# Optimization experiments

Measured on AMD Instinct MI355X. Metric: run time of the kernel, lower is better.

The kernel has to match this reference:

```python
import jax, jax.numpy as jnp
import numpy as np

IN_DIM, OUT_DIM = 256, 64
N_D, N_G, N_C, N_S = 100000, 50000, 50000, 20000
E = 1000000
ALPHA = 0.2  # LeakyReLU negative slope


def setup_inputs() -> dict:
    key = jax.random.key(0)
    ks = jax.random.split(key, 14)
    scale = float(np.sqrt(6.0 / (IN_DIM + OUT_DIM)) * 1.414)
    scale_w = float(np.sqrt(6.0 / (4 * OUT_DIM + OUT_DIM)) * 1.414)
    return {
        "disease_feats": jax.random.normal(ks[0], (N_D, IN_DIM), jnp.float32),
        "gene_feats": jax.random.normal(ks[1], (N_G, IN_DIM), jnp.float32),
        "chemical_feats": jax.random.normal(ks[2], (N_C, IN_DIM), jnp.float32),
        "species_feats": jax.random.normal(ks[3], (N_S, IN_DIM), jnp.float32),
        "P_disease": jax.random.uniform(ks[4], (IN_DIM, OUT_DIM), jnp.float32, -scale, scale),
        "P_gene": jax.random.uniform(ks[5], (IN_DIM, OUT_DIM), jnp.float32, -scale, scale),
        "P_chemical": jax.random.uniform(ks[6], (IN_DIM, OUT_DIM), jnp.float32, -scale, scale),
        "P_species": jax.random.uniform(ks[7], (IN_DIM, OUT_DIM), jnp.float32, -scale, scale),
        "W_GDCD": jax.random.uniform(ks[8], (4 * OUT_DIM, OUT_DIM), jnp.float32, -scale_w, scale_w),
        "idx_d0": jax.random.randint(ks[9], (E,), 0, N_D, jnp.int32),
        "idx_d1": jax.random.randint(ks[10], (E,), 0, N_D, jnp.int32),
        "idx_g": jax.random.randint(ks[11], (E,), 0, N_G, jnp.int32),
        "idx_c": jax.random.randint(ks[12], (E,), 0, N_C, jnp.int32),
    }


def reference(disease_feats, gene_feats, chemical_feats, species_feats,
              P_disease, P_gene, P_chemical, P_species, W_GDCD,
              idx_d0, idx_d1, idx_g, idx_c):
    # Per-type linear projections (pattern 'GDCD')
    f_disease = disease_feats @ P_disease      # [N_D, out]
    f_gene = gene_feats @ P_gene               # [N_G, out]
    f_chemical = chemical_feats @ P_chemical   # [N_C, out]
    # f_species is computed by the torch code but unused for GDCD; omitted (dead code under jit)
    # Gather per-instance rows and concat -> [E, 4*out]
    concat = jnp.concatenate(
        [f_disease[idx_d0], f_disease[idx_d1], f_gene[idx_g], f_chemical[idx_c]], axis=1)
    instance = concat @ W_GDCD                 # [E, out]
    return jax.nn.leaky_relu(instance, negative_slope=ALPHA)
```

## Files before the change

kernel.cpp:

```cpp
#include <hip/hip_runtime.h>

typedef __attribute__((ext_vector_type(8))) short          short8;
typedef __attribute__((ext_vector_type(4))) float          f32x4;
typedef __attribute__((ext_vector_type(8))) unsigned short ushort8;

#define ALPHA 0.2f

__device__ __forceinline__ unsigned short f2bf(float f) {
    union { float f; unsigned int u; } x; x.f = f;
    unsigned int u = x.u;
    u += 0x7fffu + ((u >> 16) & 1u);
    return (unsigned short)(u >> 16);
}
__device__ __forceinline__ float bf2f(unsigned short u) {
    union { unsigned int i; float f; } x; x.i = ((unsigned int)u) << 16;
    return x.f;
}

__global__ __launch_bounds__(256)
void make_frags(const float* __restrict__ Pd, const float* __restrict__ Pg,
                const float* __restrict__ Pc, const float* __restrict__ W,
                unsigned short* __restrict__ fd, unsigned short* __restrict__ fg,
                unsigned short* __restrict__ fc) {
    int t = blockIdx.x * 256 + threadIdx.x;
    int local, NCT, mbase; unsigned short* dst;
    if (t < 32768)      { local = t;         NCT = 8; dst = fd; mbase = 0; }
    else if (t < 49152) { local = t - 32768; NCT = 4; dst = fg; mbase = 2; }
    else                { local = t - 49152; NCT = 4; dst = fc; mbase = 3; }
    int j    = local & 7;
    int lane = (local >> 3) & 63;
    int ct   = (local >> 9) & (NCT - 1);
    int kk   = local >> (9 + (NCT == 8 ? 3 : 2));
    int k = kk * 32 + ((lane >> 4) << 3) + j;
    int c = ct * 16 + (lane & 15);
    int m, cc; const float* P;
    if (NCT == 8) { m = (c < 64) ? 0 : 1; cc = c & 63; P = Pd; }
    else          { m = mbase;            cc = c;      P = (mbase == 2) ? Pg : Pc; }
    float acc = 0.f;
    #pragma unroll 8
    for (int q = 0; q < 64; ++q)
        acc += P[k * 64 + q] * W[(m * 64 + q) * 64 + cc];
    dst[local] = f2bf(acc);
}

#define TPW 2

template <int NCT>
__device__ __forceinline__
void proj_body(const float* __restrict__ feats,
               const unsigned short* __restrict__ bfrag,
               unsigned short* __restrict__ g, int ntiles, int blk,
               unsigned short* blds) {
    const int t = threadIdx.x;
    #pragma unroll
    for (int i = 0; i < NCT; ++i) {
        int off = (i * 512 + t) * 8;
        *(int4*)&blds[off] = *(const int4*)&bfrag[off];
    }
    __syncthreads();

    const int wid = t >> 6, lane = t & 63;
    const int C = NCT * 16;

    #pragma unroll
    for (int it = 0; it < TPW; ++it) {
        const int tile = (blk * 8 + wid) * TPW + it;
        if (tile >= ntiles) return;

        const int row = tile * 16 + (lane & 15);
        const float* arow = feats + (size_t)row * 256 + ((lane >> 4) * 8);

        f32x4 acc[NCT];
        #pragma unroll
        for (int ct = 0; ct < NCT; ++ct) acc[ct] = (f32x4){0.f, 0.f, 0.f, 0.f};

        #pragma unroll
        for (int kk = 0; kk < 8; ++kk) {
            f32x4 v0 = __builtin_nontemporal_load((const f32x4*)(arow + kk * 32));
            f32x4 v1 = __builtin_nontemporal_load((const f32x4*)(arow + kk * 32 + 4));
            short8 a;
            a[0] = (short)f2bf(v0[0]); a[1] = (short)f2bf(v0[1]);
            a[2] = (short)f2bf(v0[2]); a[3] = (short)f2bf(v0[3]);
            a[4] = (short)f2bf(v1[0]); a[5] = (short)f2bf(v1[1]);
            a[6] = (short)f2bf(v1[2]); a[7] = (short)f2bf(v1[3]);
            #pragma unroll
            for (int ct = 0; ct < NCT; ++ct) {
                short8 b = *(const short8*)&blds[((kk * NCT + ct) * 64 + lane) * 8];
                acc[ct] = __builtin_amdgcn_mfma_f32_16x16x32_bf16(a, b, acc[ct], 0, 0, 0);
            }
        }

        const int rbase = tile * 16 + (lane >> 4) * 4;
        const int cbase = lane & 15;
        #pragma unroll
        for (int ct = 0; ct < NCT; ++ct) {
            #pragma unroll
            for (int j = 0; j < 4; ++j)
                g[(size_t)(rbase + j) * C + ct * 16 + cbase] = f2bf(acc[ct][j]);
        }
    }
}

__global__ __launch_bounds__(512)
void proj_all(const float* __restrict__ featd, const float* __restrict__ featg,
              const float* __restrict__ featc,
              const unsigned short* __restrict__ fragd,
              const unsigned short* __restrict__ fragg,
              const unsigned short* __restrict__ fragc,
              unsigned short* __restrict__ g_d, unsigned short* __restrict__ g_g,
              unsigned short* __restrict__ g_c,
              int nbd, int nbg, int td, int tg, int tc) {
    __shared__ unsigned short blds[32768];
    int b = blockIdx.x;
    if (b < nbd)            proj_body<8>(featd, fragd, g_d, td, b,             blds);
    else if (b < nbd + nbg) proj_body<4>(featg, fragg, g_g, tg, b - nbd,       blds);
    else                    proj_body<4>(featc, fragc, g_c, tc, b - nbd - nbg, blds);
}

__global__ __launch_bounds__(256)
void gather_kernel(const unsigned short* __restrict__ g_d,
                   const unsigned short* __restrict__ g_g,
                   const unsigned short* __restrict__ g_c,
                   const int* __restrict__ i0, const int* __restrict__ i1,
                   const int* __restrict__ ig, const int* __restrict__ ic,
                   float* __restrict__ out, int E, int Eh) {
    int tid = blockIdx.x * 256 + threadIdx.x;
    int e0 = tid >> 3;
    if (e0 >= Eh) return;
    int q = tid & 3;
    q = tid & 7;
    int e1 = e0 + Eh;
    bool has1 = e1 < E;

    int a0  = __builtin_nontemporal_load(i0 + e0);
    int b0  = __builtin_nontemporal_load(i1 + e0);
    int gi0 = __builtin_nontemporal_load(ig + e0);
    int ci0 = __builtin_nontemporal_load(ic + e0);
    int a1 = 0, b1 = 0, gi1 = 0, ci1 = 0;
    if (has1) {
        a1  = __builtin_nontemporal_load(i0 + e1);
        b1  = __builtin_nontemporal_load(i1 + e1);
        gi1 = __builtin_nontemporal_load(ig + e1);
        ci1 = __builtin_nontemporal_load(ic + e1);
    }

    ushort8 v0 = *(const ushort8*)(g_d + (size_t)a0  * 128 + q * 8);
    ushort8 v1 = *(const ushort8*)(g_d + (size_t)b0  * 128 + 64 + q * 8);
    ushort8 v2 = *(const ushort8*)(g_g + (size_t)gi0 * 64 + q * 8);
    ushort8 v3 = *(const ushort8*)(g_c + (size_t)ci0 * 64 + q * 8);
    ushort8 w0, w1, w2, w3;
    if (has1) {
        w0 = *(const ushort8*)(g_d + (size_t)a1  * 128 + q * 8);
        w1 = *(const ushort8*)(g_d + (size_t)b1  * 128 + 64 + q * 8);
        w2 = *(const ushort8*)(g_g + (size_t)gi1 * 64 + q * 8);
        w3 = *(const ushort8*)(g_c + (size_t)ci1 * 64 + q * 8);
    }

    f32x4 r0, r1;
    #pragma unroll
    for (int j = 0; j < 4; ++j) {
        float s = bf2f(v0[j]) + bf2f(v1[j]) + bf2f(v2[j]) + bf2f(v3[j]);
        r0[j] = s >= 0.f ? s : s * ALPHA;
        float u = bf2f(v0[j + 4]) + bf2f(v1[j + 4]) + bf2f(v2[j + 4]) + bf2f(v3[j + 4]);
        r1[j] = u >= 0.f ? u : u * ALPHA;
    }
    float* o0 = out + (size_t)e0 * 64 + q * 8;
    __builtin_nontemporal_store(r0, (f32x4*)o0);
    __builtin_nontemporal_store(r1, (f32x4*)(o0 + 4));

    if (has1) {
        #pragma unroll
        for (int j = 0; j < 4; ++j) {
            float s = bf2f(w0[j]) + bf2f(w1[j]) + bf2f(w2[j]) + bf2f(w3[j]);
            r0[j] = s >= 0.f ? s : s * ALPHA;
            float u = bf2f(w0[j + 4]) + bf2f(w1[j + 4]) + bf2f(w2[j + 4]) + bf2f(w3[j + 4]);
            r1[j] = u >= 0.f ? u : u * ALPHA;
        }
        float* o1 = out + (size_t)e1 * 64 + q * 8;
        __builtin_nontemporal_store(r0, (f32x4*)o1);
        __builtin_nontemporal_store(r1, (f32x4*)(o1 + 4));
    }
}

extern "C" void kernel_launch(void* const* d_in, const int* in_sizes, int n_in,
                              void* d_out, int out_size, void* d_ws, size_t ws_size,
                              hipStream_t stream) {
    const float* feats_d = (const float*)d_in[0];
    const float* feats_g = (const float*)d_in[1];
    const float* feats_c = (const float*)d_in[2];
    const float* Pd = (const float*)d_in[4];
    const float* Pg = (const float*)d_in[5];
    const float* Pc = (const float*)d_in[6];
    const float* W  = (const float*)d_in[8];
    const int* i0 = (const int*)d_in[9];
    const int* i1 = (const int*)d_in[10];
    const int* ig = (const int*)d_in[11];
    const int* ic = (const int*)d_in[12];
    float* out = (float*)d_out;

    const int N_D = in_sizes[0] / 256;
    const int N_G = in_sizes[1] / 256;
    const int N_C = in_sizes[2] / 256;
    const int E   = in_sizes[9];

    char* ws = (char*)d_ws;
    unsigned short* fd  = (unsigned short*)ws;
    unsigned short* fg  = (unsigned short*)(ws + 65536);
    unsigned short* fc  = (unsigned short*)(ws + 98304);
    unsigned short* g_d = (unsigned short*)(ws + 131072);
    unsigned short* g_g = g_d + (size_t)N_D * 128;
    unsigned short* g_c = g_g + (size_t)N_G * 64;

    make_frags<<<256, 256, 0, stream>>>(Pd, Pg, Pc, W, fd, fg, fc);

    int td = N_D / 16, tg = N_G / 16, tc = N_C / 16;
    int nbd = (td + 8 * TPW - 1) / (8 * TPW);
    int nbg = (tg + 8 * TPW - 1) / (8 * TPW);
    int nbc = (tc + 8 * TPW - 1) / (8 * TPW);
    proj_all<<<nbd + nbg + nbc, 512, 0, stream>>>(
        feats_d, feats_g, feats_c, fd, fg, fc, g_d, g_g, g_c,
        nbd, nbg, td, tg, tc);

    int Eh = (E + 1) / 2;
    long long nthreads = (long long)Eh * 8;
    gather_kernel<<<(int)((nthreads + 255) / 256), 256, 0, stream>>>(
        g_d, g_g, g_c, i0, i1, ig, ic, out, E, Eh);
}
```

Baseline: 201.5 us.

## Use one tile per wave in projection, adjacent edge pairs in gather, library bf16 convert

The projection kernel drops the two-tiles-per-wave loop, so each wave handles a single 16-row tile and twice as many blocks are launched, each reloading the B fragments into LDS. Feature loads switch from nontemporal to normal loads. The gather kernel now processes adjacent edge pairs (2p, 2p+1) instead of edges split by half the range, which changes index and output locality. The hand-written float-to-bf16 rounding is replaced with the HIP library conversion.

```diff
diff --git a/kernel.cpp b/kernel.cpp
--- a/kernel.cpp
+++ b/kernel.cpp
@@ -1,4 +1,5 @@
 #include <hip/hip_runtime.h>
+#include <hip/hip_bf16.h>
 
 typedef __attribute__((ext_vector_type(8))) short          short8;
 typedef __attribute__((ext_vector_type(4))) float          f32x4;
@@ -7,10 +8,9 @@
 #define ALPHA 0.2f
 
 __device__ __forceinline__ unsigned short f2bf(float f) {
-    union { float f; unsigned int u; } x; x.f = f;
-    unsigned int u = x.u;
-    u += 0x7fffu + ((u >> 16) & 1u);
-    return (unsigned short)(u >> 16);
+    union { __hip_bfloat16 b; unsigned short u; } cv;
+    cv.b = __float2bfloat16(f);
+    return cv.u;
 }
 __device__ __forceinline__ float bf2f(unsigned short u) {
     union { unsigned int i; float f; } x; x.i = ((unsigned int)u) << 16;
@@ -43,8 +43,6 @@
     dst[local] = f2bf(acc);
 }
 
-#define TPW 2
-
 template <int NCT>
 __device__ __forceinline__
 void proj_body(const float* __restrict__ feats,
@@ -61,43 +59,39 @@
 
     const int wid = t >> 6, lane = t & 63;
     const int C = NCT * 16;
-
-    #pragma unroll
-    for (int it = 0; it < TPW; ++it) {
-        const int tile = (blk * 8 + wid) * TPW + it;
-        if (tile >= ntiles) return;
-
-        const int row = tile * 16 + (lane & 15);
-        const float* arow = feats + (size_t)row * 256 + ((lane >> 4) * 8);
-
-        f32x4 acc[NCT];
-        #pragma unroll
-        for (int ct = 0; ct < NCT; ++ct) acc[ct] = (f32x4){0.f, 0.f, 0.f, 0.f};
-
-        #pragma unroll
-        for (int kk = 0; kk < 8; ++kk) {
-            f32x4 v0 = __builtin_nontemporal_load((const f32x4*)(arow + kk * 32));
-            f32x4 v1 = __builtin_nontemporal_load((const f32x4*)(arow + kk * 32 + 4));
-            short8 a;
-            a[0] = (short)f2bf(v0[0]); a[1] = (short)f2bf(v0[1]);
-            a[2] = (short)f2bf(v0[2]); a[3] = (short)f2bf(v0[3]);
-            a[4] = (short)f2bf(v1[0]); a[5] = (short)f2bf(v1[1]);
-            a[6] = (short)f2bf(v1[2]); a[7] = (short)f2bf(v1[3]);
-            #pragma unroll
-            for (int ct = 0; ct < NCT; ++ct) {
-                short8 b = *(const short8*)&blds[((kk * NCT + ct) * 64 + lane) * 8];
-                acc[ct] = __builtin_amdgcn_mfma_f32_16x16x32_bf16(a, b, acc[ct], 0, 0, 0);
-            }
-        }
-
-        const int rbase = tile * 16 + (lane >> 4) * 4;
-        const int cbase = lane & 15;
+    const int tile = blk * 8 + wid;
+    if (tile >= ntiles) return;
+
+    const int row = tile * 16 + (lane & 15);
+    const float* arow = feats + (size_t)row * 256 + ((lane >> 4) * 8);
+
+    f32x4 acc[NCT];
+    #pragma unroll
+    for (int ct = 0; ct < NCT; ++ct) acc[ct] = (f32x4){0.f, 0.f, 0.f, 0.f};
+
+    #pragma unroll
+    for (int kk = 0; kk < 8; ++kk) {
+        f32x4 v0 = *(const f32x4*)(arow + kk * 32);
+        f32x4 v1 = *(const f32x4*)(arow + kk * 32 + 4);
+        short8 a;
+        a[0] = (short)f2bf(v0[0]); a[1] = (short)f2bf(v0[1]);
+        a[2] = (short)f2bf(v0[2]); a[3] = (short)f2bf(v0[3]);
+        a[4] = (short)f2bf(v1[0]); a[5] = (short)f2bf(v1[1]);
+        a[6] = (short)f2bf(v1[2]); a[7] = (short)f2bf(v1[3]);
         #pragma unroll
         for (int ct = 0; ct < NCT; ++ct) {
-            #pragma unroll
-            for (int j = 0; j < 4; ++j)
-                g[(size_t)(rbase + j) * C + ct * 16 + cbase] = f2bf(acc[ct][j]);
+            short8 b = *(const short8*)&blds[((kk * NCT + ct) * 64 + lane) * 8];
+            acc[ct] = __builtin_amdgcn_mfma_f32_16x16x32_bf16(a, b, acc[ct], 0, 0, 0);
         }
+    }
+
+    const int rbase = tile * 16 + (lane >> 4) * 4;
+    const int cbase = lane & 15;
+    #pragma unroll
+    for (int ct = 0; ct < NCT; ++ct) {
+        #pragma unroll
+        for (int j = 0; j < 4; ++j)
+            g[(size_t)(rbase + j) * C + ct * 16 + cbase] = f2bf(acc[ct][j]);
     }
 }
 
@@ -123,26 +117,22 @@
                    const unsigned short* __restrict__ g_c,
                    const int* __restrict__ i0, const int* __restrict__ i1,
                    const int* __restrict__ ig, const int* __restrict__ ic,
-                   float* __restrict__ out, int E, int Eh) {
+                   float* __restrict__ out, int E) {
     int tid = blockIdx.x * 256 + threadIdx.x;
-    int e0 = tid >> 3;
-    if (e0 >= Eh) return;
-    int q = tid & 3;
-    q = tid & 7;
-    int e1 = e0 + Eh;
+    int p = tid >> 3;
+    int q = tid & 7;
+    int e0 = p * 2, e1 = p * 2 + 1;
+    if (e0 >= E) return;
     bool has1 = e1 < E;
 
     int a0  = __builtin_nontemporal_load(i0 + e0);
     int b0  = __builtin_nontemporal_load(i1 + e0);
     int gi0 = __builtin_nontemporal_load(ig + e0);
     int ci0 = __builtin_nontemporal_load(ic + e0);
-    int a1 = 0, b1 = 0, gi1 = 0, ci1 = 0;
-    if (has1) {
-        a1  = __builtin_nontemporal_load(i0 + e1);
-        b1  = __builtin_nontemporal_load(i1 + e1);
-        gi1 = __builtin_nontemporal_load(ig + e1);
-        ci1 = __builtin_nontemporal_load(ic + e1);
-    }
+    int a1  = has1 ? __builtin_nontemporal_load(i0 + e1) : 0;
+    int b1  = has1 ? __builtin_nontemporal_load(i1 + e1) : 0;
+    int gi1 = has1 ? __builtin_nontemporal_load(ig + e1) : 0;
+    int ci1 = has1 ? __builtin_nontemporal_load(ic + e1) : 0;
 
     ushort8 v0 = *(const ushort8*)(g_d + (size_t)a0  * 128 + q * 8);
     ushort8 v1 = *(const ushort8*)(g_d + (size_t)b0  * 128 + 64 + q * 8);
@@ -214,15 +204,13 @@
     make_frags<<<256, 256, 0, stream>>>(Pd, Pg, Pc, W, fd, fg, fc);
 
     int td = N_D / 16, tg = N_G / 16, tc = N_C / 16;
-    int nbd = (td + 8 * TPW - 1) / (8 * TPW);
-    int nbg = (tg + 8 * TPW - 1) / (8 * TPW);
-    int nbc = (tc + 8 * TPW - 1) / (8 * TPW);
+    int nbd = (td + 7) / 8, nbg = (tg + 7) / 8, nbc = (tc + 7) / 8;
     proj_all<<<nbd + nbg + nbc, 512, 0, stream>>>(
         feats_d, feats_g, feats_c, fd, fg, fc, g_d, g_g, g_c,
         nbd, nbg, td, tg, tc);
 
-    int Eh = (E + 1) / 2;
-    long long nthreads = (long long)Eh * 8;
+    int pairs = (E + 1) / 2;
+    long long nthreads = (long long)pairs * 8;
     gather_kernel<<<(int)((nthreads + 255) / 256), 256, 0, stream>>>(
-        g_d, g_g, g_c, i0, i1, ig, ic, out, E, Eh);
-}
+        g_d, g_g, g_c, i0, i1, ig, ic, out, E);
+}
```

After: 171.9 us. -14.7%, faster.
